# Optimization experiments

Measured on AMD Instinct MI355X. Metric: run time of the kernel, lower is better.

The kernel has to match this reference:

```python
import jax, jax.numpy as jnp
import numpy as np

B, C, H, W = 4, 256, 64, 64
N = H * W


def _c1(Wt, x, b=None):
    # 1x1 conv2d: Wt [out,in], x [B,in,H,W]
    r = jnp.einsum('oi,bihw->bohw', Wt, x)
    return r if b is None else r + b[None, :, None, None]


def setup_inputs() -> dict:
    key = jax.random.key(0)
    ks = jax.random.split(key, 32)
    s = 0.01  # torch init: normal(0, 0.01)
    d = {
        'x': jax.random.normal(ks[0], (B, C, H, W), jnp.float32),
        'y': jax.random.normal(ks[1], (B, C, H, W), jnp.float32),
        'z': jax.random.normal(ks[2], (B, C, 6, 6), jnp.float32),
        'm': jax.random.normal(ks[3], (B, C, 3, 3), jnp.float32),
        'Wv':  jax.random.normal(ks[4], (C, C), jnp.float32) * s,   # conv_value, no bias
        'Wv2': jax.random.normal(ks[5], (C, C), jnp.float32) * s,   # conv_value_2, no bias
        'Wq':  jax.random.normal(ks[6], (C, C), jnp.float32) * s,
        'bq':  jnp.zeros((C,), jnp.float32),
        'Wk':  jax.random.normal(ks[7], (C, C), jnp.float32) * s,
        'bk':  jnp.zeros((C,), jnp.float32),
        'Wq2': jax.random.normal(ks[8], (C, C), jnp.float32) * s,
        'bq2': jnp.zeros((C,), jnp.float32),
        'Wk2': jax.random.normal(ks[9], (C, C), jnp.float32) * s,
        'bk2': jnp.zeros((C,), jnp.float32),
        'Win1': jax.random.normal(ks[10], (C, C), jnp.float32) * s,
        'bin1': jnp.zeros((C,), jnp.float32),
        'Win3': jax.random.normal(ks[11], (C, C), jnp.float32) * s,
        'bin3': jnp.zeros((C,), jnp.float32),
        'Wtr':  jax.random.normal(ks[12], (2 * C, 2 * C), jnp.float32) * s,
        'btr':  jnp.zeros((2 * C,), jnp.float32),
        'Wout2': jax.random.normal(ks[13], (C, C), jnp.float32) * s,
        'bout2': jnp.zeros((C,), jnp.float32),
        'Wout3': jax.random.normal(ks[14], (C, C), jnp.float32) * s,
        'bout3': jnp.zeros((C,), jnp.float32),
        'Wfc': jax.random.normal(ks[15], (36, 9), jnp.float32) * (1.0 / 3.0),  # nn.Linear(9,36)
        'bfc': jnp.zeros((36,), jnp.float32),
        # gammas init to 0 in torch, which zeroes the attention branch; use
        # nonzero values so the baseline exercises the full graph.
        'gamma':  jnp.full((1,), 0.5, jnp.float32),
        'gamma2': jnp.full((1,), 0.5, jnp.float32),
    }
    return d


def reference(x, y, z, m, Wv, Wv2, Wq, bq, Wk, bk, Wq2, bq2, Wk2, bk2,
              Win1, bin1, Win3, bin3, Wtr, btr, Wout2, bout2, Wout3, bout3,
              Wfc, bfc, gamma, gamma2):
    Bs, Cc, Hh, Ww = x.shape
    Nn = Hh * Ww
    # conv_value on y, z, m (no bias)
    yv = _c1(Wv, y)
    zv = _c1(Wv, z)
    mv = _c1(Wv, m)
    y_line = yv.reshape(Bs, Cc, Nn)            # [B,C,N]
    z_line = zv.reshape(Bs, Cc, 36)            # [B,C,36]
    m_line = mv.reshape(Bs, Cc, 9) @ Wfc.T + bfc   # [B,C,36]
    m_line = jnp.transpose(m_line, (0, 2, 1))      # [B,36,C]
    fuse_mz = jnp.einsum('bcn,bnd->bcd', z_line, m_line)      # [B,C,C]
    fuse_mzy = jnp.einsum('bcd,bdn->bcn', fuse_mz, y_line).reshape(yv.shape) + yv  # [B,C,H,W]

    value = fuse_mzy.reshape(Bs, Cc, Nn)                      # [B,C,N]
    value_2 = _c1(Wv2, x).reshape(Bs, Cc, Nn)
    query = _c1(Wq, x, bq).reshape(Bs, Cc, Nn)
    key = _c1(Wk, fuse_mzy, bk).reshape(Bs, Cc, Nn)
    query_2 = _c1(Wq2, x, bq2).reshape(Bs, Cc, Nn)
    key_2 = _c1(Wk2, x, bk2).reshape(Bs, Cc, Nn)

    # branch 1: Q^T K -> softmax over keys -> @ V^T
    sim = jax.nn.softmax(jnp.einsum('bcn,bcm->bnm', query, key), axis=2)
    out_sim = jnp.einsum('bnm,bcm->bcn', sim, value).reshape(Bs, Cc, Hh, Ww)
    out_sim = gamma[0] * out_sim

    # branch 2
    sim2 = jax.nn.softmax(jnp.einsum('bcn,bcm->bnm', query_2, key_2), axis=2)
    out_sim_2 = jnp.einsum('bnm,bcm->bcn', sim2, value_2).reshape(Bs, Cc, Hh, Ww)
    out_sim_2 = gamma2[0] * out_sim_2

    # sigmoid-gated fusion
    H_1 = _c1(Win1, out_sim, bin1)
    H_3 = _c1(Win3, out_sim_2, bin3)
    H_tra = _c1(Wtr, jnp.concatenate([H_1, H_3], axis=1), btr)
    H_5 = jax.nn.sigmoid(_c1(Wout2, H_tra[:, :Cc], bout2))
    H_6 = jax.nn.sigmoid(_c1(Wout3, H_tra[:, Cc:], bout3))
    H_all = jax.nn.softmax(jnp.stack([H_5, H_6], axis=0), axis=0)
    return H_all[0] * out_sim + H_all[1] * out_sim_2 + x
```

## Files before the change

### kernel.cpp

```cpp
#include <hip/hip_runtime.h>

typedef unsigned short u16;
typedef int   v4i __attribute__((ext_vector_type(4)));
typedef float v4f __attribute__((ext_vector_type(4)));

__device__ __forceinline__ float b2f(u16 v) {
    union { unsigned u; float f; } t; t.u = ((unsigned)v) << 16; return t.f;
}
__device__ __forceinline__ u16 f2b(float f) {
    union { float f; unsigned u; } t; t.f = f;
    unsigned r = (t.u + 0x7FFFu + ((t.u >> 16) & 1u)) >> 16;
    return (u16)r;
}
__device__ __forceinline__ u16 f2b_trunc(float f) {
    union { float f; unsigned u; } t; t.f = f;
    return (u16)(t.u >> 16);
}
__device__ __forceinline__ v4f mfma16(v4i a, v4i b, v4f c) {
    asm("v_mfma_f32_16x16x32_bf16 %0, %1, %2, %0" : "+v"(c) : "v"(a), "v"(b));
    return c;
}
__device__ __forceinline__ void gload16(const u16* g, u16* l) {
    __builtin_amdgcn_global_load_lds(
        (const __attribute__((address_space(1))) unsigned int*)g,
        (__attribute__((address_space(3))) unsigned int*)l,
        16, 0, 0);
}

struct WCvt { const float* s[6]; u16* d[6]; };
__global__ void cvt_weights(WCvt p) {
    int wi = blockIdx.y;
    int i = blockIdx.x * 256 + threadIdx.x;
    p.d[wi][i] = f2b(p.s[wi][i]);
}

__global__ void wprod1(const float* __restrict__ Wtr, const float* __restrict__ Win1,
                       const float* __restrict__ Win3, const float* __restrict__ bin1,
                       const float* __restrict__ bin3, const float* __restrict__ btr,
                       float* __restrict__ T, float* __restrict__ btr_eff)
{
    const int y = blockIdx.y, i = blockIdx.x, j = threadIdx.x;
    if (i == 256) {
        if (y != 0) return;
        float s0 = btr[j], s1 = btr[256 + j];
        for (int k = 0; k < 256; k++) {
            s0 += Wtr[(long)j * 512 + k] * bin1[k] + Wtr[(long)j * 512 + 256 + k] * bin3[k];
            s1 += Wtr[(long)(256 + j) * 512 + k] * bin1[k] + Wtr[(long)(256 + j) * 512 + 256 + k] * bin3[k];
        }
        btr_eff[j] = s0; btr_eff[256 + j] = s1;
        return;
    }
    const int row = (y >= 2) ? 256 + i : i;
    const int coff = (y & 1) ? 256 : 0;
    const float* W2 = (y & 1) ? Win3 : Win1;
    __shared__ float wrow[256];
    wrow[j] = Wtr[(long)row * 512 + coff + j];
    __syncthreads();
    float s = 0.f;
    for (int k = 0; k < 256; k++) s += wrow[k] * W2[k * 256 + j];
    T[((long)y * 256 + i) * 256 + j] = s;
}

__global__ void wprod2(const float* __restrict__ Wout2, const float* __restrict__ Wout3,
                       const float* __restrict__ bout2, const float* __restrict__ bout3,
                       const float* __restrict__ T, const float* __restrict__ btr_eff,
                       u16* __restrict__ PQ, float* __restrict__ r5, float* __restrict__ r6)
{
    const int y = blockIdx.y, i = blockIdx.x, j = threadIdx.x;
    if (i == 256) {
        if (y == 0) {
            float s = bout2[j];
            for (int k = 0; k < 256; k++) s += Wout2[(long)j * 256 + k] * btr_eff[k];
            r5[j] = s;
        } else if (y == 2) {
            float s = bout3[j];
            for (int k = 0; k < 256; k++) s += Wout3[(long)j * 256 + k] * btr_eff[256 + k];
            r6[j] = s;
        }
        return;
    }
    const float* Wo = (y >= 2) ? Wout3 : Wout2;
    __shared__ float wrow[256];
    wrow[j] = Wo[(long)i * 256 + j];
    __syncthreads();
    const float* Ty = T + (long)y * 65536;
    float s = 0.f;
    for (int k = 0; k < 256; k++) s += wrow[k] * Ty[k * 256 + j];
    PQ[((long)y * 256 + i) * 256 + j] = f2b(s);
}

__global__ __launch_bounds__(256) void transpose_cvt(
    const float* __restrict__ x, const float* __restrict__ y,
    u16* __restrict__ xt, u16* __restrict__ yt)
{
    const int z = blockIdx.z, t = z >> 2, b = z & 3;
    const float* src = t ? y : x;
    u16* dst = t ? yt : xt;
    __shared__ float tile[32][33];
    const int nt = blockIdx.x * 32, ct = blockIdx.y * 32;
    const int tx = threadIdx.x, ty = threadIdx.y;
#pragma unroll
    for (int i = 0; i < 4; i++)
        tile[ty + i * 8][tx] = src[((long)b * 256 + ct + ty + i * 8) * 4096 + nt + tx];
    __syncthreads();
#pragma unroll
    for (int i = 0; i < 4; i++)
        dst[((long)b * 4096 + nt + ty + i * 8) * 256 + ct + tx] = f2b(tile[tx][ty + i * 8]);
}

__global__ void small_zm(const float* __restrict__ z, const float* __restrict__ m,
                         const float* __restrict__ Wv, const float* __restrict__ Wfc,
                         const float* __restrict__ bfc,
                         float* __restrict__ zv, float* __restrict__ mline)
{
    const int o = blockIdx.x, b = blockIdx.y, tid = threadIdx.x;
    __shared__ float wrow[256];
    __shared__ float mvs[9];
    for (int i = tid; i < 256; i += 64) wrow[i] = Wv[o * 256 + i];
    __syncthreads();
    if (tid < 36) {
        float s = 0.f;
        for (int c = 0; c < 256; c++) s += wrow[c] * z[((long)b * 256 + c) * 36 + tid];
        zv[((long)b * 256 + o) * 36 + tid] = s;
    }
    if (tid < 9) {
        float s = 0.f;
        for (int c = 0; c < 256; c++) s += wrow[c] * m[((long)b * 256 + c) * 9 + tid];
        mvs[tid] = s;
    }
    __syncthreads();
    if (tid < 36) {
        float s = bfc[tid];
        for (int k = 0; k < 9; k++) s += mvs[k] * Wfc[tid * 9 + k];
        mline[((long)b * 256 + o) * 36 + tid] = s;
    }
}

__global__ void small_F(const float* __restrict__ zv, const float* __restrict__ mline,
                        u16* __restrict__ Fb, u16* __restrict__ FbT)
{
    const int c = blockIdx.x, b = blockIdx.y, d = threadIdx.x;
    const float* zr = zv + ((long)b * 256 + c) * 36;
    const float* mr = mline + ((long)b * 256 + d) * 36;
    float s = (c == d) ? 1.f : 0.f;
    for (int n = 0; n < 36; n++) s += zr[n] * mr[n];
    u16 v = f2b(s);
    Fb[((long)b * 256 + c) * 256 + d] = v;
    FbT[((long)b * 256 + d) * 256 + c] = v;
}

struct GDesc {
    const u16* X; const u16* W; const float* bias;
    u16* outT; u16* outN;
    long xbs, wbs, otbs, onbs;
    int ldx, ldw, ldot, ldon, K, rows;
};
struct GJob { GDesc d[8]; int oblk; };

__global__ __launch_bounds__(256) void gemm_tn(GJob j) {
    const int di = blockIdx.y / j.oblk;
    const int o0 = (blockIdx.y % j.oblk) * 128;
    const GDesc g = j.d[di];
    const int b = blockIdx.z;
    const int n0 = blockIdx.x * 128;
    if (n0 >= g.rows) return;
    const int tid = threadIdx.x, lane = tid & 63, w = tid >> 6;
    const int l15 = lane & 15, lg = lane >> 4;
    const int wr = (w >> 1) * 64, wc = (w & 1) * 64;
    const u16* Xp = g.X + b * g.xbs + (long)(n0 + wr + l15) * g.ldx + lg * 8;
    const u16* Wp = g.W + b * g.wbs + (long)(o0 + wc + l15) * g.ldw + lg * 8;

    v4f acc[4][4];
    for (int oi = 0; oi < 4; oi++) {
        float bv = g.bias ? g.bias[o0 + wc + oi * 16 + l15] : 0.f;
        for (int mi = 0; mi < 4; mi++) acc[mi][oi] = (v4f){bv, bv, bv, bv};
    }
#pragma unroll 4
    for (int k = 0; k < g.K; k += 32) {
        v4i a[4], bb[4];
#pragma unroll
        for (int mi = 0; mi < 4; mi++) a[mi] = *(const v4i*)(Xp + (long)mi * 16 * g.ldx + k);
#pragma unroll
        for (int oi = 0; oi < 4; oi++) bb[oi] = *(const v4i*)(Wp + (long)oi * 16 * g.ldw + k);
#pragma unroll
        for (int mi = 0; mi < 4; mi++)
#pragma unroll
            for (int oi = 0; oi < 4; oi++)
                acc[mi][oi] = mfma16(a[mi], bb[oi], acc[mi][oi]);
    }
    for (int mi = 0; mi < 4; mi++)
        for (int oi = 0; oi < 4; oi++) {
            int nn = n0 + wr + mi * 16 + lg * 4;
            int oo = o0 + wc + oi * 16 + l15;
            if (g.outT) {
                u16* p = g.outT + b * g.otbs + (long)nn * g.ldot + oo;
#pragma unroll
                for (int r = 0; r < 4; r++) p[(long)r * g.ldot] = f2b(acc[mi][oi][r]);
            }
            if (g.outN) {
                ushort4 pk;
                pk.x = f2b(acc[mi][oi][0]); pk.y = f2b(acc[mi][oi][1]);
                pk.z = f2b(acc[mi][oi][2]); pk.w = f2b(acc[mi][oi][3]);
                *(ushort4*)(g.outN + b * g.onbs + (long)oo * g.ldon + nn) = pk;
            }
        }
}

__global__ __launch_bounds__(256) void attn_kernel(
    const u16* __restrict__ qtA, const u16* __restrict__ ktA, const u16* __restrict__ vA,
    u16* __restrict__ otA, u16* __restrict__ onA, const float* __restrict__ gA,
    const u16* __restrict__ qtB, const u16* __restrict__ ktB, const u16* __restrict__ vB,
    u16* __restrict__ otB, u16* __restrict__ onB, const float* __restrict__ gB)
{
    const int wg = blockIdx.x;
    const int qb = wg >> 3, code = wg & 7;
    const int br = code & 1, b = code >> 1;
    const u16* Qt = br ? qtB : qtA;
    const u16* Kt = br ? ktB : ktA;
    const u16* V  = br ? vB  : vA;
    u16* Ot = br ? otB : otA;
    u16* On = br ? onB : onA;
    const float gamma = br ? gB[0] : gA[0];
    const long bs = (long)4096 * 256;
    const u16* Qb = Qt + b * bs;
    const u16* Kb = Kt + b * bs;
    const u16* Vb = V + b * bs;
    u16* Otb = Ot + b * bs;
    u16* Onb = On + b * bs;

    const int tid = threadIdx.x, lane = tid & 63, w = tid >> 6;
    const int l15 = lane & 15, lg = lane >> 4;

    __shared__ __align__(16) u16 Ksh[4][8192];
    __shared__ __align__(16) u16 P[2][64][56];
    __shared__ float den[64];

    v4i qf[8];
    const u16* qp = Qb + (long)(qb * 64 + w * 16 + l15) * 256 + lg * 8;
#pragma unroll
    for (int ks = 0; ks < 8; ks++) qf[ks] = *(const v4i*)(qp + ks * 32);

    v4f oacc[4][4];
    for (int ci = 0; ci < 4; ci++)
        for (int qi = 0; qi < 4; qi++) oacc[ci][qi] = (v4f){0.f, 0.f, 0.f, 0.f};
    float dacc[4] = {0.f, 0.f, 0.f, 0.f};

    const u16* vb = Vb + (long)(w * 64 + l15) * 4096 + lg * 8;
    v4i vfA[4], vfB[4];

    const int srow = w * 8 + (lane >> 5);
    const int scolB = (lane & 31) * 16;

    auto STAGE = [&](int buf, int t) {
        const u16* base = Kb + (long)t * 8192;
        u16* lb = &Ksh[buf][w * 2048];
#pragma unroll
        for (int i = 0; i < 4; i++) {
            int row = srow + i * 2;
            int colB = scolB ^ ((row & 7) << 4);
            gload16(base + row * 256 + (colB >> 1), lb + i * 512);
        }
    };
    auto VLOAD = [&](v4i (&vf)[4], int t) {
#pragma unroll
        for (int ci = 0; ci < 4; ci++)
            vf[ci] = *(const v4i*)(vb + (long)ci * 16 * 4096 + t * 32);
    };

    STAGE(0, 0);
    STAGE(1, 1);
    STAGE(2, 2);
    VLOAD(vfA, 0);
    asm volatile("s_waitcnt vmcnt(12)" ::: "memory");
    __builtin_amdgcn_s_barrier();
    __builtin_amdgcn_sched_barrier(0);

    auto ITER = [&](int mb, v4i (&vcur)[4], v4i (&vnxt)[4]) {
        const u16* kb = &Ksh[mb & 3][0];
        u16* Pc = &P[mb & 1][0][0];

        v4f l0a = {0,0,0,0}, l0b = {0,0,0,0}, l1a = {0,0,0,0}, l1b = {0,0,0,0};
        __builtin_amdgcn_s_setprio(1);
#pragma unroll
        for (int ks = 0; ks < 4; ks++) {
            int c0 = (ks * 64 + lg * 16) ^ ((l15 & 7) << 4);
            v4i k0 = *(const v4i*)(kb + l15 * 256 + (c0 >> 1));
            v4i k1 = *(const v4i*)(kb + (16 + l15) * 256 + (c0 >> 1));
            l0a = mfma16(qf[ks], k0, l0a);
            l1a = mfma16(qf[ks], k1, l1a);
        }
#pragma unroll
        for (int ks = 4; ks < 8; ks++) {
            int c0 = (ks * 64 + lg * 16) ^ ((l15 & 7) << 4);
            v4i k0 = *(const v4i*)(kb + l15 * 256 + (c0 >> 1));
            v4i k1 = *(const v4i*)(kb + (16 + l15) * 256 + (c0 >> 1));
            l0b = mfma16(qf[ks], k0, l0b);
            l1b = mfma16(qf[ks], k1, l1b);
        }
        __builtin_amdgcn_s_setprio(0);
        v4f lacc0 = l0a + l0b, lacc1 = l1a + l1b;

#pragma unroll
        for (int r = 0; r < 4; r++) {
            float e0 = __expf(lacc0[r]);
            float e1 = __expf(lacc1[r]);
            dacc[r] += e0 + e1;
            Pc[(w * 16 + lg * 4 + r) * 56 + l15]      = f2b_trunc(e0);
            Pc[(w * 16 + lg * 4 + r) * 56 + 16 + l15] = f2b_trunc(e1);
        }

        if (mb < 127) VLOAD(vnxt, mb + 1);
        if (mb < 125) STAGE((mb + 3) & 3, mb + 3);

        if (mb <= 124)      asm volatile("s_waitcnt vmcnt(16) lgkmcnt(0)" ::: "memory");
        else if (mb == 125) asm volatile("s_waitcnt vmcnt(12) lgkmcnt(0)" ::: "memory");
        else if (mb == 126) asm volatile("s_waitcnt vmcnt(8) lgkmcnt(0)" ::: "memory");
        else                asm volatile("s_waitcnt vmcnt(0) lgkmcnt(0)" ::: "memory");
        __builtin_amdgcn_s_barrier();
        __builtin_amdgcn_sched_barrier(0);

        v4i pf[4];
#pragma unroll
        for (int qi = 0; qi < 4; qi++)
            pf[qi] = *(const v4i*)(Pc + (qi * 16 + l15) * 56 + lg * 8);
        __builtin_amdgcn_s_setprio(1);
#pragma unroll
        for (int ci = 0; ci < 4; ci++)
#pragma unroll
            for (int qi = 0; qi < 4; qi++)
                oacc[ci][qi] = mfma16(vcur[ci], pf[qi], oacc[ci][qi]);
        __builtin_amdgcn_s_setprio(0);
    };

    for (int mb2 = 0; mb2 < 64; ++mb2) {
        ITER(2 * mb2,     vfA, vfB);
        ITER(2 * mb2 + 1, vfB, vfA);
    }

#pragma unroll
    for (int r = 0; r < 4; r++) {
        float s = dacc[r];
        s += __shfl_xor(s, 1); s += __shfl_xor(s, 2);
        s += __shfl_xor(s, 4); s += __shfl_xor(s, 8);
        if (l15 == 0) den[w * 16 + lg * 4 + r] = s;
    }
    __syncthreads();

    for (int qi = 0; qi < 4; qi++) {
        int q = qi * 16 + l15;
        float sc = gamma / den[q];
        int n = qb * 64 + q;
        for (int ci = 0; ci < 4; ci++) {
            int c0 = w * 64 + ci * 16 + lg * 4;
            ushort4 pk;
            pk.x = f2b(oacc[ci][qi][0] * sc);
            pk.y = f2b(oacc[ci][qi][1] * sc);
            pk.z = f2b(oacc[ci][qi][2] * sc);
            pk.w = f2b(oacc[ci][qi][3] * sc);
            *(ushort4*)(Otb + (long)n * 256 + c0) = pk;
            Onb[(long)(c0 + 0) * 4096 + n] = pk.x;
            Onb[(long)(c0 + 1) * 4096 + n] = pk.y;
            Onb[(long)(c0 + 2) * 4096 + n] = pk.z;
            Onb[(long)(c0 + 3) * 4096 + n] = pk.w;
        }
    }
}

__global__ __launch_bounds__(256) void gate2_gemm(
    const u16* __restrict__ Ot, const u16* __restrict__ O2t,
    const u16* __restrict__ PQ, const float* __restrict__ r5, const float* __restrict__ r6,
    const u16* __restrict__ On, const u16* __restrict__ O2n,
    const float* __restrict__ x, float* __restrict__ out)
{
    const int bz = blockIdx.z;
    const int n0 = blockIdx.x * 64, c0 = blockIdx.y * 64;
    const int tid = threadIdx.x, lane = tid & 63, w = tid >> 6;
    const int l15 = lane & 15, lg = lane >> 4;
    const int wr = (w >> 1) * 32, wc = (w & 1) * 32;
    const long NC = 4096L * 256;
    const u16* Xa = Ot + bz * NC + (long)(n0 + wr + l15) * 256 + lg * 8;
    const u16* Xb = O2t + bz * NC + (long)(n0 + wr + l15) * 256 + lg * 8;
    const long crow = c0 + wc + l15;
    const u16* W5a = PQ + crow * 256 + lg * 8;
    const u16* W5b = PQ + 65536 + crow * 256 + lg * 8;
    const u16* W6a = PQ + 131072 + crow * 256 + lg * 8;
    const u16* W6b = PQ + 196608 + crow * 256 + lg * 8;

    v4f a5[2][2], a6[2][2];
    for (int oi = 0; oi < 2; oi++) {
        float v5 = r5[c0 + wc + oi * 16 + l15];
        float v6 = r6[c0 + wc + oi * 16 + l15];
        for (int mi = 0; mi < 2; mi++) {
            a5[mi][oi] = (v4f){v5, v5, v5, v5};
            a6[mi][oi] = (v4f){v6, v6, v6, v6};
        }
    }
#pragma unroll 4
    for (int k = 0; k < 256; k += 32) {
        v4i xa[2], w5[2], w6[2];
#pragma unroll
        for (int mi = 0; mi < 2; mi++) xa[mi] = *(const v4i*)(Xa + (long)mi * 16 * 256 + k);
#pragma unroll
        for (int oi = 0; oi < 2; oi++) {
            w5[oi] = *(const v4i*)(W5a + (long)oi * 16 * 256 + k);
            w6[oi] = *(const v4i*)(W6a + (long)oi * 16 * 256 + k);
        }
#pragma unroll
        for (int mi = 0; mi < 2; mi++)
#pragma unroll
            for (int oi = 0; oi < 2; oi++) {
                a5[mi][oi] = mfma16(xa[mi], w5[oi], a5[mi][oi]);
                a6[mi][oi] = mfma16(xa[mi], w6[oi], a6[mi][oi]);
            }
    }
#pragma unroll 4
    for (int k = 0; k < 256; k += 32) {
        v4i xa[2], w5[2], w6[2];
#pragma unroll
        for (int mi = 0; mi < 2; mi++) xa[mi] = *(const v4i*)(Xb + (long)mi * 16 * 256 + k);
#pragma unroll
        for (int oi = 0; oi < 2; oi++) {
            w5[oi] = *(const v4i*)(W5b + (long)oi * 16 * 256 + k);
            w6[oi] = *(const v4i*)(W6b + (long)oi * 16 * 256 + k);
        }
#pragma unroll
        for (int mi = 0; mi < 2; mi++)
#pragma unroll
            for (int oi = 0; oi < 2; oi++) {
                a5[mi][oi] = mfma16(xa[mi], w5[oi], a5[mi][oi]);
                a6[mi][oi] = mfma16(xa[mi], w6[oi], a6[mi][oi]);
            }
    }
    for (int mi = 0; mi < 2; mi++)
        for (int oi = 0; oi < 2; oi++) {
            int n = n0 + wr + mi * 16 + lg * 4;
            int c = c0 + wc + oi * 16 + l15;
            long base = (long)c * 4096 + n;
            ushort4 ov  = *(const ushort4*)(On + bz * NC + base);
            ushort4 ov2 = *(const ushort4*)(O2n + bz * NC + base);
            float4 xv = *(const float4*)(x + ((long)bz * 256 + c) * 4096 + n);
            u16 av[4] = {ov.x, ov.y, ov.z, ov.w};
            u16 cv[4] = {ov2.x, ov2.y, ov2.z, ov2.w};
            float xr[4] = {xv.x, xv.y, xv.z, xv.w};
            float o[4];
#pragma unroll
            for (int r = 0; r < 4; r++) {
                float s5 = 1.f / (1.f + __expf(-a5[mi][oi][r]));
                float s6 = 1.f / (1.f + __expf(-a6[mi][oi][r]));
                float w0 = 1.f / (1.f + __expf(s6 - s5));
                o[r] = w0 * b2f(av[r]) + (1.f - w0) * b2f(cv[r]) + xr[r];
            }
            *(float4*)(out + ((long)bz * 256 + c) * 4096 + n) = make_float4(o[0], o[1], o[2], o[3]);
        }
}

extern "C" void kernel_launch(void* const* d_in, const int* in_sizes, int n_in,
                              void* d_out, int out_size, void* d_ws, size_t ws_size,
                              hipStream_t stream)
{
    const float* x     = (const float*)d_in[0];
    const float* y     = (const float*)d_in[1];
    const float* z     = (const float*)d_in[2];
    const float* m     = (const float*)d_in[3];
    const float* Wv    = (const float*)d_in[4];
    const float* Wv2   = (const float*)d_in[5];
    const float* Wq    = (const float*)d_in[6];
    const float* bq    = (const float*)d_in[7];
    const float* Wk    = (const float*)d_in[8];
    const float* bk    = (const float*)d_in[9];
    const float* Wq2   = (const float*)d_in[10];
    const float* bq2   = (const float*)d_in[11];
    const float* Wk2   = (const float*)d_in[12];
    const float* bk2   = (const float*)d_in[13];
    const float* Win1  = (const float*)d_in[14];
    const float* bin1  = (const float*)d_in[15];
    const float* Win3  = (const float*)d_in[16];
    const float* bin3  = (const float*)d_in[17];
    const float* Wtr   = (const float*)d_in[18];
    const float* btr   = (const float*)d_in[19];
    const float* Wout2 = (const float*)d_in[20];
    const float* bout2 = (const float*)d_in[21];
    const float* Wout3 = (const float*)d_in[22];
    const float* bout3 = (const float*)d_in[23];
    const float* Wfc   = (const float*)d_in[24];
    const float* bfc   = (const float*)d_in[25];
    const float* gamma  = (const float*)d_in[26];
    const float* gamma2 = (const float*)d_in[27];

    char* ws = (char*)d_ws;
    u16* Wb[6];
    for (int i = 0; i < 6; i++) Wb[i] = (u16*)(ws + (size_t)i * 131072);
    u16* Gk   = (u16*)(ws + 786432);
    u16* Fb   = (u16*)(ws + 1310720);
    u16* FbT  = (u16*)(ws + 1835008);
    u16* PQ   = (u16*)(ws + 2359296);
    float* T  = (float*)(ws + 2883584);
    float* zv    = (float*)(ws + 2883584);
    float* mline = (float*)(ws + 2883584 + 147456);
    float* btr_eff = (float*)(ws + 3932160);
    float* r5 = (float*)(ws + 3934208);
    float* r6 = (float*)(ws + 3935232);
    auto SLOT = [&](int i) { return ws + 4194304 + (size_t)i * 8388608; };
    u16* xt  = (u16*)SLOT(0);
    u16* yt  = (u16*)SLOT(1);
    u16* yvt = (u16*)SLOT(2);
    u16* fmn = (u16*)SLOT(4);
    u16* v2n = (u16*)SLOT(5);
    u16* qt  = (u16*)SLOT(6);
    u16* kt  = (u16*)SLOT(7);
    u16* q2t = (u16*)SLOT(8);
    u16* k2t = (u16*)SLOT(9);
    u16* O2n = (u16*)SLOT(0);
    u16* Ot_ = (u16*)SLOT(1);
    u16* On_ = (u16*)SLOT(2);
    u16* O2t = (u16*)SLOT(3);

    const long NC = 4096L * 256, CC = 65536;

    WCvt wc;
    const float* wsrc[6] = {Wv, Wv2, Wq, Wk, Wq2, Wk2};
    for (int i = 0; i < 6; i++) { wc.s[i] = wsrc[i]; wc.d[i] = Wb[i]; }
    cvt_weights<<<dim3(256, 6), 256, 0, stream>>>(wc);

    wprod1<<<dim3(257, 4), 256, 0, stream>>>(Wtr, Win1, Win3, bin1, bin3, btr, T, btr_eff);
    wprod2<<<dim3(257, 4), 256, 0, stream>>>(Wout2, Wout3, bout2, bout3, T, btr_eff, PQ, r5, r6);

    transpose_cvt<<<dim3(128, 8, 8), dim3(32, 8), 0, stream>>>(x, y, xt, yt);

    small_zm<<<dim3(256, 4), 64, 0, stream>>>(z, m, Wv, Wfc, bfc, zv, mline);
    small_F<<<dim3(256, 4), 256, 0, stream>>>(zv, mline, Fb, FbT);

    auto mkdesc = [](const u16* X, int ldx, long xbs, const u16* W, int ldw, long wbs,
                     const float* bias, u16* outT, int ldot, long otbs,
                     u16* outN, int ldon, long onbs, int K, int rows) {
        GDesc g; g.X = X; g.W = W; g.bias = bias; g.outT = outT; g.outN = outN;
        g.xbs = xbs; g.wbs = wbs; g.otbs = otbs; g.onbs = onbs;
        g.ldx = ldx; g.ldw = ldw; g.ldot = ldot; g.ldon = ldon; g.K = K; g.rows = rows;
        return g;
    };

    {
        GJob j{}; j.oblk = 2;
        j.d[0] = mkdesc(yt, 256, NC, Wb[0], 256, 0, nullptr, yvt, 256, NC, nullptr, 0, 0, 256, 4096);
        j.d[1] = mkdesc(xt, 256, NC, Wb[2], 256, 0, bq,  qt,  256, NC, nullptr, 0, 0, 256, 4096);
        j.d[2] = mkdesc(xt, 256, NC, Wb[4], 256, 0, bq2, q2t, 256, NC, nullptr, 0, 0, 256, 4096);
        j.d[3] = mkdesc(xt, 256, NC, Wb[5], 256, 0, bk2, k2t, 256, NC, nullptr, 0, 0, 256, 4096);
        j.d[4] = mkdesc(xt, 256, NC, Wb[1], 256, 0, nullptr, nullptr, 0, 0, v2n, 4096, NC, 256, 4096);
        j.d[5] = mkdesc(Wb[3], 256, 0, FbT, 256, CC, nullptr, Gk, 256, CC, nullptr, 0, 0, 256, 256);
        gemm_tn<<<dim3(32, 12, 4), 256, 0, stream>>>(j);
    }
    {
        GJob j{}; j.oblk = 2;
        j.d[0] = mkdesc(yvt, 256, NC, Fb, 256, CC, nullptr, nullptr, 0, 0, fmn, 4096, NC, 256, 4096);
        j.d[1] = mkdesc(yvt, 256, NC, Gk, 256, CC, bk, kt, 256, NC, nullptr, 0, 0, 256, 4096);
        gemm_tn<<<dim3(32, 4, 4), 256, 0, stream>>>(j);
    }

    attn_kernel<<<dim3(512), 256, 0, stream>>>(qt, kt, fmn, Ot_, On_, gamma,
                                               q2t, k2t, v2n, O2t, O2n, gamma2);

    gate2_gemm<<<dim3(64, 4, 4), 256, 0, stream>>>(Ot_, O2t, PQ, r5, r6,
                                                   On_, O2n, x, (float*)d_out);
}
```

Before: 404.8 us.

## Widen attention key tiles to 64 with double buffering, transpose gate GEMM operands

The attention kernel now processes 64 keys per iteration instead of 32, with 2 K buffers instead of 4 and a single P tile, so there are half as many iterations and barriers. Each iteration issues more MFMAs, at the cost of more registers and shallower prefetch. The gate GEMM swaps its operands so that channels map to MFMA rows. Its epilogue now does scalar loads and stores per element rather than float4 along n, which is intended to give coalescing across lanes but drops the vector width.

```diff
diff --git a/kernel.cpp b/kernel.cpp
--- a/kernel.cpp
+++ b/kernel.cpp
@@ -231,8 +231,8 @@
     const int tid = threadIdx.x, lane = tid & 63, w = tid >> 6;
     const int l15 = lane & 15, lg = lane >> 4;
 
-    __shared__ __align__(16) u16 Ksh[4][8192];
-    __shared__ __align__(16) u16 P[2][64][56];
+    __shared__ __align__(16) u16 Ksh[2][16384];
+    __shared__ __align__(16) u16 P[64][72];
     __shared__ float den[64];
 
     v4i qf[8];
@@ -246,95 +246,116 @@
     float dacc[4] = {0.f, 0.f, 0.f, 0.f};
 
     const u16* vb = Vb + (long)(w * 64 + l15) * 4096 + lg * 8;
-    v4i vfA[4], vfB[4];
-
-    const int srow = w * 8 + (lane >> 5);
+    v4i vfA[4][2], vfB[4][2];
+
+    const int srow = w * 16 + (lane >> 5);
     const int scolB = (lane & 31) * 16;
 
     auto STAGE = [&](int buf, int t) {
-        const u16* base = Kb + (long)t * 8192;
-        u16* lb = &Ksh[buf][w * 2048];
-#pragma unroll
-        for (int i = 0; i < 4; i++) {
+        const u16* base = Kb + (long)t * 16384;
+        u16* lb = &Ksh[buf][w * 4096];
+#pragma unroll
+        for (int i = 0; i < 8; i++) {
             int row = srow + i * 2;
             int colB = scolB ^ ((row & 7) << 4);
             gload16(base + row * 256 + (colB >> 1), lb + i * 512);
         }
     };
-    auto VLOAD = [&](v4i (&vf)[4], int t) {
+    auto VLOAD = [&](v4i (&vf)[4][2], int t) {
 #pragma unroll
         for (int ci = 0; ci < 4; ci++)
-            vf[ci] = *(const v4i*)(vb + (long)ci * 16 * 4096 + t * 32);
+#pragma unroll
+            for (int ks = 0; ks < 2; ks++)
+                vf[ci][ks] = *(const v4i*)(vb + (long)ci * 16 * 4096 + t * 64 + ks * 32);
     };
 
     STAGE(0, 0);
-    STAGE(1, 1);
-    STAGE(2, 2);
+    __builtin_amdgcn_sched_barrier(0);
     VLOAD(vfA, 0);
-    asm volatile("s_waitcnt vmcnt(12)" ::: "memory");
+    asm volatile("s_waitcnt vmcnt(8)" ::: "memory");
     __builtin_amdgcn_s_barrier();
     __builtin_amdgcn_sched_barrier(0);
 
-    auto ITER = [&](int mb, v4i (&vcur)[4], v4i (&vnxt)[4]) {
-        const u16* kb = &Ksh[mb & 3][0];
-        u16* Pc = &P[mb & 1][0][0];
-
-        v4f l0a = {0,0,0,0}, l0b = {0,0,0,0}, l1a = {0,0,0,0}, l1b = {0,0,0,0};
+    auto ITER = [&](int t, v4i (&vcur)[4][2], v4i (&vnxt)[4][2]) {
+        const int cur = t & 1;
+        const u16* kb = &Ksh[cur][0];
+
+        if (t < 63) STAGE(cur ^ 1, t + 1);
+        __builtin_amdgcn_sched_barrier(0);
+
+        v4f la[4], lb2[4];
+#pragma unroll
+        for (int mi = 0; mi < 4; mi++) { la[mi] = (v4f){0,0,0,0}; lb2[mi] = (v4f){0,0,0,0}; }
         __builtin_amdgcn_s_setprio(1);
 #pragma unroll
         for (int ks = 0; ks < 4; ks++) {
             int c0 = (ks * 64 + lg * 16) ^ ((l15 & 7) << 4);
-            v4i k0 = *(const v4i*)(kb + l15 * 256 + (c0 >> 1));
-            v4i k1 = *(const v4i*)(kb + (16 + l15) * 256 + (c0 >> 1));
-            l0a = mfma16(qf[ks], k0, l0a);
-            l1a = mfma16(qf[ks], k1, l1a);
+#pragma unroll
+            for (int mi = 0; mi < 4; mi++) {
+                v4i kf = *(const v4i*)(kb + (mi * 16 + l15) * 256 + (c0 >> 1));
+                la[mi] = mfma16(qf[ks], kf, la[mi]);
+            }
         }
 #pragma unroll
         for (int ks = 4; ks < 8; ks++) {
             int c0 = (ks * 64 + lg * 16) ^ ((l15 & 7) << 4);
-            v4i k0 = *(const v4i*)(kb + l15 * 256 + (c0 >> 1));
-            v4i k1 = *(const v4i*)(kb + (16 + l15) * 256 + (c0 >> 1));
-            l0b = mfma16(qf[ks], k0, l0b);
-            l1b = mfma16(qf[ks], k1, l1b);
+#pragma unroll
+            for (int mi = 0; mi < 4; mi++) {
+                v4i kf = *(const v4i*)(kb + (mi * 16 + l15) * 256 + (c0 >> 1));
+                lb2[mi] = mfma16(qf[ks], kf, lb2[mi]);
+            }
         }
         __builtin_amdgcn_s_setprio(0);
-        v4f lacc0 = l0a + l0b, lacc1 = l1a + l1b;
-
-#pragma unroll
-        for (int r = 0; r < 4; r++) {
-            float e0 = __expf(lacc0[r]);
-            float e1 = __expf(lacc1[r]);
-            dacc[r] += e0 + e1;
-            Pc[(w * 16 + lg * 4 + r) * 56 + l15]      = f2b_trunc(e0);
-            Pc[(w * 16 + lg * 4 + r) * 56 + 16 + l15] = f2b_trunc(e1);
-        }
-
-        if (mb < 127) VLOAD(vnxt, mb + 1);
-        if (mb < 125) STAGE((mb + 3) & 3, mb + 3);
-
-        if (mb <= 124)      asm volatile("s_waitcnt vmcnt(16) lgkmcnt(0)" ::: "memory");
-        else if (mb == 125) asm volatile("s_waitcnt vmcnt(12) lgkmcnt(0)" ::: "memory");
-        else if (mb == 126) asm volatile("s_waitcnt vmcnt(8) lgkmcnt(0)" ::: "memory");
-        else                asm volatile("s_waitcnt vmcnt(0) lgkmcnt(0)" ::: "memory");
+
+        if (t < 63) VLOAD(vnxt, t + 1);
+
+        u16 pw[4][4];
+#pragma unroll
+        for (int mi = 0; mi < 4; mi++) {
+            v4f l = la[mi] + lb2[mi];
+#pragma unroll
+            for (int r = 0; r < 4; r++) {
+                float e = __expf(l[r]);
+                dacc[r] += e;
+                pw[mi][r] = f2b_trunc(e);
+            }
+        }
+
+        __builtin_amdgcn_sched_barrier(0);
         __builtin_amdgcn_s_barrier();
         __builtin_amdgcn_sched_barrier(0);
 
-        v4i pf[4];
+#pragma unroll
+        for (int mi = 0; mi < 4; mi++)
+#pragma unroll
+            for (int r = 0; r < 4; r++)
+                P[w * 16 + lg * 4 + r][mi * 16 + l15] = pw[mi][r];
+
+        if (t < 63) asm volatile("s_waitcnt vmcnt(8) lgkmcnt(0)" ::: "memory");
+        else        asm volatile("s_waitcnt vmcnt(0) lgkmcnt(0)" ::: "memory");
+        __builtin_amdgcn_s_barrier();
+        __builtin_amdgcn_sched_barrier(0);
+
+        v4i pf[4][2];
 #pragma unroll
         for (int qi = 0; qi < 4; qi++)
-            pf[qi] = *(const v4i*)(Pc + (qi * 16 + l15) * 56 + lg * 8);
+#pragma unroll
+            for (int ks = 0; ks < 2; ks++)
+                pf[qi][ks] = *(const v4i*)(&P[qi * 16 + l15][ks * 32 + lg * 8]);
         __builtin_amdgcn_s_setprio(1);
 #pragma unroll
-        for (int ci = 0; ci < 4; ci++)
-#pragma unroll
-            for (int qi = 0; qi < 4; qi++)
-                oacc[ci][qi] = mfma16(vcur[ci], pf[qi], oacc[ci][qi]);
+        for (int ks = 0; ks < 2; ks++)
+#pragma unroll
+            for (int ci = 0; ci < 4; ci++)
+#pragma unroll
+                for (int qi = 0; qi < 4; qi++)
+                    oacc[ci][qi] = mfma16(vcur[ci][ks], pf[qi][ks], oacc[ci][qi]);
         __builtin_amdgcn_s_setprio(0);
     };
 
-    for (int mb2 = 0; mb2 < 64; ++mb2) {
-        ITER(2 * mb2,     vfA, vfB);
-        ITER(2 * mb2 + 1, vfB, vfA);
+    for (int t2 = 0; t2 < 32; ++t2) {
+        ITER(2 * t2,     vfA, vfB);
+        ITER(2 * t2 + 1, vfB, vfA);
     }
 
 #pragma unroll
@@ -376,82 +397,81 @@
     const int n0 = blockIdx.x * 64, c0 = blockIdx.y * 64;
     const int tid = threadIdx.x, lane = tid & 63, w = tid >> 6;
     const int l15 = lane & 15, lg = lane >> 4;
-    const int wr = (w >> 1) * 32, wc = (w & 1) * 32;
+    const int wcc = (w >> 1) * 32, wnn = (w & 1) * 32;
     const long NC = 4096L * 256;
-    const u16* Xa = Ot + bz * NC + (long)(n0 + wr + l15) * 256 + lg * 8;
-    const u16* Xb = O2t + bz * NC + (long)(n0 + wr + l15) * 256 + lg * 8;
-    const long crow = c0 + wc + l15;
-    const u16* W5a = PQ + crow * 256 + lg * 8;
-    const u16* W5b = PQ + 65536 + crow * 256 + lg * 8;
-    const u16* W6a = PQ + 131072 + crow * 256 + lg * 8;
-    const u16* W6b = PQ + 196608 + crow * 256 + lg * 8;
+    const long arow = c0 + wcc + l15;
+    const u16* pa5 = PQ + arow * 256 + lg * 8;
+    const u16* qa5 = PQ + 65536 + arow * 256 + lg * 8;
+    const u16* pa6 = PQ + 131072 + arow * 256 + lg * 8;
+    const u16* qa6 = PQ + 196608 + arow * 256 + lg * 8;
+    const u16* bo  = Ot  + bz * NC + (long)(n0 + wnn + l15) * 256 + lg * 8;
+    const u16* bo2 = O2t + bz * NC + (long)(n0 + wnn + l15) * 256 + lg * 8;
 
     v4f a5[2][2], a6[2][2];
-    for (int oi = 0; oi < 2; oi++) {
-        float v5 = r5[c0 + wc + oi * 16 + l15];
-        float v6 = r6[c0 + wc + oi * 16 + l15];
-        for (int mi = 0; mi < 2; mi++) {
-            a5[mi][oi] = (v4f){v5, v5, v5, v5};
-            a6[mi][oi] = (v4f){v6, v6, v6, v6};
-        }
-    }
+    for (int mi = 0; mi < 2; mi++)
+        for (int oi = 0; oi < 2; oi++) {
+            a5[mi][oi] = (v4f){0, 0, 0, 0};
+            a6[mi][oi] = (v4f){0, 0, 0, 0};
+        }
 #pragma unroll 4
     for (int k = 0; k < 256; k += 32) {
-        v4i xa[2], w5[2], w6[2];
-#pragma unroll
-        for (int mi = 0; mi < 2; mi++) xa[mi] = *(const v4i*)(Xa + (long)mi * 16 * 256 + k);
-#pragma unroll
-        for (int oi = 0; oi < 2; oi++) {
-            w5[oi] = *(const v4i*)(W5a + (long)oi * 16 * 256 + k);
-            w6[oi] = *(const v4i*)(W6a + (long)oi * 16 * 256 + k);
+        v4i bb[2], w5[2], w6[2];
+#pragma unroll
+        for (int oi = 0; oi < 2; oi++) bb[oi] = *(const v4i*)(bo + (long)oi * 16 * 256 + k);
+#pragma unroll
+        for (int mi = 0; mi < 2; mi++) {
+            w5[mi] = *(const v4i*)(pa5 + (long)mi * 16 * 256 + k);
+            w6[mi] = *(const v4i*)(pa6 + (long)mi * 16 * 256 + k);
         }
 #pragma unroll
         for (int mi = 0; mi < 2; mi++)
 #pragma unroll
             for (int oi = 0; oi < 2; oi++) {
-                a5[mi][oi] = mfma16(xa[mi], w5[oi], a5[mi][oi]);
-                a6[mi][oi] = mfma16(xa[mi], w6[oi], a6[mi][oi]);
+                a5[mi][oi] = mfma16(w5[mi], bb[oi], a5[mi][oi]);
+                a6[mi][oi] = mfma16(w6[mi], bb[oi], a6[mi][oi]);
             }
     }
 #pragma unroll 4
     for (int k = 0; k < 256; k += 32) {
-        v4i xa[2], w5[2], w6[2];
-#pragma unroll
-        for (int mi = 0; mi < 2; mi++) xa[mi] = *(const v4i*)(Xb + (long)mi * 16 * 256 + k);
-#pragma unroll
+        v4i bb[2], w5[2], w6[2];
+#pragma unroll
+        for (int oi = 0; oi < 2; oi++) bb[oi] = *(const v4i*)(bo2 + (long)oi * 16 * 256 + k);
+#pragma unroll
+        for (int mi = 0; mi < 2; mi++) {
+            w5[mi] = *(const v4i*)(qa5 + (long)mi * 16 * 256 + k);
+            w6[mi] = *(const v4i*)(qa6 + (long)mi * 16 * 256 + k);
+        }
+#pragma unroll
+        for (int mi = 0; mi < 2; mi++)
+#pragma unroll
+            for (int oi = 0; oi < 2; oi++) {
+                a5[mi][oi] = mfma16(w5[mi], bb[oi], a5[mi][oi]);
+                a6[mi][oi] = mfma16(w6[mi], bb[oi], a6[mi][oi]);
+            }
+    }
+    for (int mi = 0; mi < 2; mi++) {
+        float r5v[4], r6v[4];
+#pragma unroll
+        for (int r = 0; r < 4; r++) {
+            int c = c0 + wcc + mi * 16 + lg * 4 + r;
+            r5v[r] = r5[c]; r6v[r] = r6[c];
+        }
         for (int oi = 0; oi < 2; oi++) {
-            w5[oi] = *(const v4i*)(W5b + (long)oi * 16 * 256 + k);
-            w6[oi] = *(const v4i*)(W6b + (long)oi * 16 * 256 + k);
-        }
-#pragma unroll
-        for (int mi = 0; mi < 2; mi++)
-#pragma unroll
-            for (int oi = 0; oi < 2; oi++) {
-                a5[mi][oi] = mfma16(xa[mi], w5[oi], a5[mi][oi]);
-                a6[mi][oi] = mfma16(xa[mi], w6[oi], a6[mi][oi]);
-            }
-    }
-    for (int mi = 0; mi < 2; mi++)
-        for (int oi = 0; oi < 2; oi++) {
-            int n = n0 + wr + mi * 16 + lg * 4;
-            int c = c0 + wc + oi * 16 + l15;
-            long base = (long)c * 4096 + n;
-            ushort4 ov  = *(const ushort4*)(On + bz * NC + base);
-            ushort4 ov2 = *(const ushort4*)(O2n + bz * NC + base);
-            float4 xv = *(const float4*)(x + ((long)bz * 256 + c) * 4096 + n);
-            u16 av[4] = {ov.x, ov.y, ov.z, ov.w};
-            u16 cv[4] = {ov2.x, ov2.y, ov2.z, ov2.w};
-            float xr[4] = {xv.x, xv.y, xv.z, xv.w};
-            float o[4];
+            int n = n0 + wnn + oi * 16 + l15;
 #pragma unroll
             for (int r = 0; r < 4; r++) {
-                float s5 = 1.f / (1.f + __expf(-a5[mi][oi][r]));
-                float s6 = 1.f / (1.f + __expf(-a6[mi][oi][r]));
+                int c = c0 + wcc + mi * 16 + lg * 4 + r;
+                long base = bz * NC + (long)c * 4096 + n;
+                float ov  = b2f(On[base]);
+                float ov2 = b2f(O2n[base]);
+                float xv  = x[((long)bz * 256 + c) * 4096 + n];
+                float s5 = 1.f / (1.f + __expf(-(a5[mi][oi][r] + r5v[r])));
+                float s6 = 1.f / (1.f + __expf(-(a6[mi][oi][r] + r6v[r])));
                 float w0 = 1.f / (1.f + __expf(s6 - s5));
-                o[r] = w0 * b2f(av[r]) + (1.f - w0) * b2f(cv[r]) + xr[r];
-            }
-            *(float4*)(out + ((long)bz * 256 + c) * 4096 + n) = make_float4(o[0], o[1], o[2], o[3]);
-        }
+                out[((long)bz * 256 + c) * 4096 + n] = w0 * ov + (1.f - w0) * ov2 + xv;
+            }
+        }
+    }
 }
 
 extern "C" void kernel_launch(void* const* d_in, const int* in_sizes, int n_in,
```

After: 520.8 us. +28.6%, slower.
